# Performance work log

Measured on AMD Instinct MI355X. Metric: run time of the kernel, lower is better.

Reference implementation:

```python
import jax, jax.numpy as jnp
import numpy as np

B, T, V, D, OUT = 32, 100, 10000, 128, 1000
CODE_P = 0.003  # ~30 active codes per visit


def gru_dir(x3, whh, bhh, reverse):
    """x3: [B,T,3F] precomputed input-side gates (W_ih x + b_ih). PyTorch GRU math."""
    F = whh.shape[1]
    h0 = jnp.zeros((x3.shape[0], F), x3.dtype)

    def step(h, xt):
        gh = h @ whh.T + bhh
        xr, xz, xn = jnp.split(xt, 3, -1)
        hr, hz, hn = jnp.split(gh, 3, -1)
        r = jax.nn.sigmoid(xr + hr)
        z = jax.nn.sigmoid(xz + hz)
        n = jnp.tanh(xn + r * hn)
        h_new = (1.0 - z) * n + z * h
        return h_new, h_new

    _, hs = jax.lax.scan(step, h0, jnp.swapaxes(x3, 0, 1), reverse=reverse)
    return jnp.swapaxes(hs, 0, 1)  # [B,T,F]


def setup_inputs() -> dict:
    key = jax.random.key(0)
    ks = jax.random.split(key, 16)
    s = lambda k, *sh: jax.random.normal(k, sh, dtype=jnp.float32) * 0.05
    # multi-hot visits, ~0/1 with density CODE_P; force code 0 present so no all-zero visit
    x = (jax.random.uniform(ks[0], (B, T, V)) < CODE_P).astype(jnp.float32)
    x = x.at[:, :, 0].set(1.0)
    return {
        "batchdata": x,
        "emb": s(ks[1], V, D),
        "wih_f": s(ks[2], 3 * D, D), "whh_f": s(ks[3], 3 * D, D),
        "bih_f": jnp.zeros((3 * D,), jnp.float32), "bhh_f": jnp.zeros((3 * D,), jnp.float32),
        "wih_b": s(ks[4], 3 * D, D), "whh_b": s(ks[5], 3 * D, D),
        "bih_b": jnp.zeros((3 * D,), jnp.float32), "bhh_b": jnp.zeros((3 * D,), jnp.float32),
        "attn_w": s(ks[6], 2 * D, 1), "attn_b": jnp.zeros((1,), jnp.float32),
        "comb_w": s(ks[7], D, 4 * D), "comb_b": jnp.zeros((D,), jnp.float32),
        "fc_w": s(ks[8], OUT, D), "fc_b": jnp.zeros((OUT,), jnp.float32),
    }


def reference(batchdata, emb, wih_f, whh_f, bih_f, bhh_f, wih_b, whh_b, bih_b, bhh_b,
              attn_w, attn_b, comb_w, comb_b, fc_w, fc_b):
    # multihot_to_embedding: sum of embedding rows where visit==1 == multihot @ table
    e = jnp.einsum('btv,vd->btd', batchdata, emb)          # [B,T,D]
    mask = jnp.any(e != 0, axis=2)                          # [B,T]
    # DipoleLayer: bidirectional GRU (hidden=D each dir), dropout in eval mode = identity
    xf = jnp.einsum('btf,gf->btg', e, wih_f) + bih_f
    xb = jnp.einsum('btf,gf->btg', e, wih_b) + bih_b
    hf = gru_dir(xf, whh_f, bhh_f, reverse=False)
    hb = gru_dir(xb, whh_b, bhh_b, reverse=True)
    h = jnp.concatenate([hf, hb], axis=-1)                  # [B,T,2D]
    # location-based attention over timesteps
    scores = (h @ attn_w)[..., 0] + attn_b[0]               # [B,T]
    scores = jnp.where(mask, scores, jnp.float32(-1e9))
    a = jax.nn.softmax(scores, axis=-1)
    c = jnp.einsum('bt,btf->bf', a, h)                      # [B,2D] context
    last = jnp.sum(mask.astype(jnp.int32), axis=-1) - 1     # last valid visit
    h_last = h[jnp.arange(h.shape[0]), last]                # [B,2D]
    feat = jnp.tanh(jnp.concatenate([c, h_last], -1) @ comb_w.T + comb_b)  # [B,D]
    logits = feat @ fc_w.T + fc_b                           # [B,OUT]
    return logits
```

## Files before the change

### kernel.cpp

```cpp
#include <hip/hip_runtime.h>
#include <hip/hip_fp16.h>
#include <math.h>

#define BB 32
#define TT 100
#define VV 10000
#define DD 128
#define OUTN 1000
#define G3 384

__global__ __launch_bounds__(256) void k_w2h(
    const float* __restrict__ wf, const float* __restrict__ wb,
    __half* __restrict__ hf, __half* __restrict__ hb)
{
    const int i = blockIdx.x * 256 + threadIdx.x;
    hf[i] = __float2half(wf[i]);
    hb[i] = __float2half(wb[i]);
}

__global__ __launch_bounds__(256) void k_embed(
    const float* __restrict__ x, const float* __restrict__ emb,
    float* __restrict__ e, int* __restrict__ mask)
{
    const int bt  = blockIdx.x;
    const int tid = threadIdx.x;
    __shared__ int   s_cnt;
    __shared__ int   s_any;
    __shared__ int   s_idx[256];
    __shared__ float s_val[256];
    if (tid == 0) { s_cnt = 0; s_any = 0; }
    __syncthreads();

    const float4* x4 = (const float4*)(x + (size_t)bt * VV);
    for (int i = tid; i < VV / 4; i += 256) {
        float4 v = x4[i];
        if (v.x != 0.f) { int p = atomicAdd(&s_cnt, 1); if (p < 256) { s_idx[p] = 4*i+0; s_val[p] = v.x; } }
        if (v.y != 0.f) { int p = atomicAdd(&s_cnt, 1); if (p < 256) { s_idx[p] = 4*i+1; s_val[p] = v.y; } }
        if (v.z != 0.f) { int p = atomicAdd(&s_cnt, 1); if (p < 256) { s_idx[p] = 4*i+2; s_val[p] = v.z; } }
        if (v.w != 0.f) { int p = atomicAdd(&s_cnt, 1); if (p < 256) { s_idx[p] = 4*i+3; s_val[p] = v.w; } }
    }
    __syncthreads();
    int cnt = s_cnt; if (cnt > 256) cnt = 256;
    if (tid < DD) {
        float a0 = 0.f, a1 = 0.f, a2 = 0.f, a3 = 0.f;
        int i = 0;
        for (; i + 3 < cnt; i += 4) {
            a0 += s_val[i+0] * emb[(size_t)s_idx[i+0] * DD + tid];
            a1 += s_val[i+1] * emb[(size_t)s_idx[i+1] * DD + tid];
            a2 += s_val[i+2] * emb[(size_t)s_idx[i+2] * DD + tid];
            a3 += s_val[i+3] * emb[(size_t)s_idx[i+3] * DD + tid];
        }
        for (; i < cnt; ++i)
            a0 += s_val[i] * emb[(size_t)s_idx[i] * DD + tid];
        float acc = (a0 + a1) + (a2 + a3);
        e[(size_t)bt * DD + tid] = acc;
        if (acc != 0.f) s_any = 1;
    }
    __syncthreads();
    if (tid == 0) mask[bt] = s_any;
}

__global__ __launch_bounds__(256) void k_gates(
    const float* __restrict__ e,
    const float* __restrict__ wih_f, const float* __restrict__ bih_f,
    const float* __restrict__ wih_b, const float* __restrict__ bih_b,
    float* __restrict__ x3)
{
    const int r0  = blockIdx.x * 8;
    const int tid = threadIdx.x;
    __shared__ __align__(16) float se[8][DD];
    for (int i = tid; i < 8 * DD; i += 256)
        se[i >> 7][i & 127] = e[(size_t)(r0 + (i >> 7)) * DD + (i & 127)];
    __syncthreads();

    for (int cc = 0; cc < 3; ++cc) {
        const int col = tid + cc * 256;
        const float* wrow;
        float bias;
        if (col < G3) { wrow = wih_f + (size_t)col * DD;        bias = bih_f[col]; }
        else          { wrow = wih_b + (size_t)(col - G3) * DD; bias = bih_b[col - G3]; }
        float acc[8];
        #pragma unroll
        for (int r = 0; r < 8; ++r) acc[r] = 0.f;
        const float4* w4 = (const float4*)wrow;
        for (int k4 = 0; k4 < DD / 4; ++k4) {
            float4 w = w4[k4];
            #pragma unroll
            for (int r = 0; r < 8; ++r) {
                float4 ev = *(const float4*)&se[r][4 * k4];
                acc[r] += ev.x * w.x + ev.y * w.y + ev.z * w.z + ev.w * w.w;
            }
        }
        #pragma unroll
        for (int r = 0; r < 8; ++r)
            x3[(size_t)(r0 + r) * 768 + col] = acc[r] + bias;
    }
}

__device__ __forceinline__ uint4 ld_pin_u128(const uint4* p)
{
    uint4 r;
    asm volatile("global_load_dwordx4 %0, %1, off" : "=v"(r) : "v"(p));
    return r;
}

typedef _Float16 h2v __attribute__((ext_vector_type(2)));
__device__ __forceinline__ h2v u2h2(unsigned u) { h2v h; __builtin_memcpy(&h, &u, 4); return h; }
__device__ __forceinline__ float2 h2f2(unsigned u)
{
    __half2 h = *reinterpret_cast<__half2*>(&u);
    return __half22float2(h);
}

#if __has_builtin(__builtin_amdgcn_fdot2)
#define DOT2(acc, wu, hu) acc = __builtin_amdgcn_fdot2(u2h2(wu), u2h2(hu), acc, false);
#else
#define DOT2(acc, wu, hu) { float2 wf_ = h2f2(wu); float2 hf_ = h2f2(hu); acc += wf_.x*hf_.x + wf_.y*hf_.y; }
#endif

__global__ __launch_bounds__(512, 1) void k_gru(
    const float* __restrict__ x3,
    const __half* __restrict__ whh16_f, const float* __restrict__ bhh_f,
    const __half* __restrict__ whh16_b, const float* __restrict__ bhh_b,
    float* __restrict__ h_all)
{
    const int dir = blockIdx.x & 1;
    const int b   = blockIdx.x >> 1;
    const int tid = threadIdx.x;
    const int g   = tid & 127;
    const int kq  = tid >> 7;
    const int kb  = kq * 32;
    const __half* whh = dir ? whh16_b : whh16_f;
    const float*  bhh = dir ? bhh_b  : bhh_f;

    const uint4* pr4 = (const uint4*)(whh + (size_t)(g         ) * DD + kb);
    const uint4* pz4 = (const uint4*)(whh + (size_t)(DD     + g) * DD + kb);
    const uint4* pn4 = (const uint4*)(whh + (size_t)(2 * DD + g) * DD + kb);

#define Q4(M) M(0) M(1) M(2) M(3)
#define DECLW(j) uint4 wr##j = ld_pin_u128(pr4 + (j)); \
                 uint4 wz##j = ld_pin_u128(pz4 + (j)); \
                 uint4 wn##j = ld_pin_u128(pn4 + (j));
    Q4(DECLW)
#undef DECLW
    asm volatile("s_waitcnt vmcnt(0)" ::: "memory");
    __builtin_amdgcn_sched_barrier(0);

    float bhr = 0.f, bhz = 0.f, bhn = 0.f;
    if (tid < DD) { bhr = bhh[g]; bhz = bhh[DD + g]; bhn = bhh[2 * DD + g]; }

    __shared__ __align__(16) __half h16[DD];
    __shared__ float p_lds[9 * DD];
    float h_reg = 0.f;
    if (tid < DD) h16[tid] = __float2half(0.f);

    float xr = 0.f, xz = 0.f, xn = 0.f;
    {
        const float* x3p = x3 + (size_t)(b * TT + (dir ? TT - 1 : 0)) * 768 + dir * G3;
        if (tid < DD) { xr = x3p[g]; xz = x3p[DD + g]; xn = x3p[2 * DD + g]; }
    }
    __syncthreads();

    for (int t = 0; t < TT; ++t) {
        const int te = dir ? (TT - 1 - t) : t;

        float nxr = 0.f, nxz = 0.f, nxn = 0.f;
        if (t + 1 < TT) {
            const int tn = dir ? (TT - 2 - t) : (t + 1);
            const float* x3n = x3 + (size_t)(b * TT + tn) * 768 + dir * G3;
            if (tid < DD) { nxr = x3n[g]; nxz = x3n[DD + g]; nxn = x3n[2 * DD + g]; }
        }

        float ar0 = 0.f, ar1 = 0.f, az0 = 0.f, az1 = 0.f, an0 = 0.f, an1 = 0.f;
#define FMA8(j) { \
        const uint4 hv = *(const uint4*)&h16[kb + 8 * (j)]; \
        DOT2(ar0, wr##j.x, hv.x) DOT2(ar1, wr##j.y, hv.y) \
        DOT2(ar0, wr##j.z, hv.z) DOT2(ar1, wr##j.w, hv.w) \
        DOT2(az0, wz##j.x, hv.x) DOT2(az1, wz##j.y, hv.y) \
        DOT2(az0, wz##j.z, hv.z) DOT2(az1, wz##j.w, hv.w) \
        DOT2(an0, wn##j.x, hv.x) DOT2(an1, wn##j.y, hv.y) \
        DOT2(an0, wn##j.z, hv.z) DOT2(an1, wn##j.w, hv.w) }
        Q4(FMA8)
#undef FMA8
        const float pr = ar0 + ar1, pz = az0 + az1, pn = an0 + an1;

        if (kq) {
            const int q = (kq - 1) * 3;
            p_lds[(q + 0) * DD + g] = pr;
            p_lds[(q + 1) * DD + g] = pz;
            p_lds[(q + 2) * DD + g] = pn;
        }
        __syncthreads();

        if (tid < DD) {
            float hr = pr + p_lds[0*DD+g] + p_lds[3*DD+g] + p_lds[6*DD+g] + bhr;
            float hz = pz + p_lds[1*DD+g] + p_lds[4*DD+g] + p_lds[7*DD+g] + bhz;
            float hn = pn + p_lds[2*DD+g] + p_lds[5*DD+g] + p_lds[8*DD+g] + bhn;
            float r  = __builtin_amdgcn_rcpf(1.f + __expf(-(xr + hr)));
            float z  = __builtin_amdgcn_rcpf(1.f + __expf(-(xz + hz)));
            float e2 = __expf(2.f * (xn + r * hn));
            float n  = 1.f - 2.f * __builtin_amdgcn_rcpf(e2 + 1.f);
            float hnew = n + z * (h_reg - n);
            h_reg = hnew;
            h16[g] = __float2half(hnew);
            h_all[(size_t)((dir * BB + b) * TT + te) * DD + g] = hnew;
        }
        __syncthreads();
        xr = nxr; xz = nxz; xn = nxn;
    }
#undef Q4
}

__global__ __launch_bounds__(256) void k_attn(
    const float* __restrict__ h_all, const int* __restrict__ mask,
    const float* __restrict__ attn_w, const float* __restrict__ attn_b,
    const float* __restrict__ comb_w, const float* __restrict__ comb_b,
    float* __restrict__ feat)
{
    const int b   = blockIdx.x;
    const int tid = threadIdx.x;
    __shared__ float s_aw[256];
    __shared__ float s_sc[128];
    __shared__ int   s_m[128];
    __shared__ float s_red[128];
    __shared__ __align__(16) float s_ch[512];

    s_aw[tid] = attn_w[tid];
    int m = 0;
    if (tid < 128) {
        m = (tid < TT) ? mask[b * TT + tid] : 0;
        s_m[tid] = m;
    }
    __syncthreads();
    for (int s = 64; s > 0; s >>= 1) {
        if (tid < s) s_m[tid] += s_m[tid + s];
        __syncthreads();
    }
    const int last = s_m[0] - 1;

    const float* hf = h_all + (size_t)(0 * BB + b) * TT * DD;
    const float* hb = h_all + (size_t)(1 * BB + b) * TT * DD;

    float sc = -1e9f;
    if (tid < TT) {
        float a = attn_b[0];
        const float4* hf4 = (const float4*)(hf + (size_t)tid * DD);
        const float4* hb4 = (const float4*)(hb + (size_t)tid * DD);
        for (int k = 0; k < DD / 4; ++k) {
            float4 v = hf4[k];
            a += v.x * s_aw[4*k] + v.y * s_aw[4*k+1] + v.z * s_aw[4*k+2] + v.w * s_aw[4*k+3];
        }
        for (int k = 0; k < DD / 4; ++k) {
            float4 v = hb4[k];
            a += v.x * s_aw[DD+4*k] + v.y * s_aw[DD+4*k+1] + v.z * s_aw[DD+4*k+2] + v.w * s_aw[DD+4*k+3];
        }
        sc = m ? a : -1e9f;
    }
    if (tid < 128) { s_sc[tid] = sc; s_red[tid] = sc; }
    __syncthreads();
    for (int s = 64; s > 0; s >>= 1) {
        if (tid < s) s_red[tid] = fmaxf(s_red[tid], s_red[tid + s]);
        __syncthreads();
    }
    const float mx = s_red[0];
    __syncthreads();
    float ex = 0.f;
    if (tid < 128) { ex = __expf(s_sc[tid] - mx); s_sc[tid] = ex; s_red[tid] = ex; }
    __syncthreads();
    for (int s = 64; s > 0; s >>= 1) {
        if (tid < s) s_red[tid] += s_red[tid + s];
        __syncthreads();
    }
    const float inv = 1.f / s_red[0];
    __syncthreads();

    {
        const int fl = tid & 127;
        const float* hp = (tid < 128) ? hf : hb;
        float csum = 0.f;
        for (int t = 0; t < TT; ++t)
            csum += s_sc[t] * hp[(size_t)t * DD + fl];
        s_ch[tid]       = csum * inv;
        s_ch[256 + tid] = hp[(size_t)last * DD + fl];
    }
    __syncthreads();

    if (tid < 128) {
        float a = comb_b[tid];
        const float4* cw = (const float4*)(comb_w + (size_t)tid * 512);
        for (int k = 0; k < 128; ++k) {
            float4 w4 = cw[k];
            float4 v4 = *(const float4*)&s_ch[4 * k];
            a += w4.x * v4.x + w4.y * v4.y + w4.z * v4.z + w4.w * v4.w;
        }
        feat[(size_t)b * DD + tid] = tanhf(a);
    }
}

__global__ __launch_bounds__(256) void k_logits(
    const float* __restrict__ feat, const float* __restrict__ fc_w,
    const float* __restrict__ fc_b, float* __restrict__ out)
{
    const int b   = blockIdx.x >> 2;
    const int oc  = blockIdx.x & 3;
    const int tid = threadIdx.x;
    const int o   = oc * 256 + tid;
    __shared__ __align__(16) float s_f[DD];
    if (tid < DD) s_f[tid] = feat[(size_t)b * DD + tid];
    __syncthreads();
    if (o < OUTN) {
        float a = fc_b[o];
        const float4* w4 = (const float4*)(fc_w + (size_t)o * DD);
        for (int k = 0; k < DD / 4; ++k) {
            float4 w = w4[k];
            float4 v = *(const float4*)&s_f[4 * k];
            a += w.x * v.x + w.y * v.y + w.z * v.z + w.w * v.w;
        }
        out[(size_t)b * OUTN + o] = a;
    }
}

extern "C" void kernel_launch(void* const* d_in, const int* in_sizes, int n_in,
                              void* d_out, int out_size, void* d_ws, size_t ws_size,
                              hipStream_t stream)
{
    const float* x      = (const float*)d_in[0];
    const float* emb    = (const float*)d_in[1];
    const float* wih_f  = (const float*)d_in[2];
    const float* whh_f  = (const float*)d_in[3];
    const float* bih_f  = (const float*)d_in[4];
    const float* bhh_f  = (const float*)d_in[5];
    const float* wih_b  = (const float*)d_in[6];
    const float* whh_b  = (const float*)d_in[7];
    const float* bih_b  = (const float*)d_in[8];
    const float* bhh_b  = (const float*)d_in[9];
    const float* attn_w = (const float*)d_in[10];
    const float* attn_b = (const float*)d_in[11];
    const float* comb_w = (const float*)d_in[12];
    const float* comb_b = (const float*)d_in[13];
    const float* fc_w   = (const float*)d_in[14];
    const float* fc_b   = (const float*)d_in[15];
    float* out = (float*)d_out;

    float*  ws      = (float*)d_ws;
    float*  e       = ws;
    float*  x3      = ws + 409600;
    float*  h_all   = ws + 2867200;
    float*  feat    = ws + 3686400;
    int*    mask    = (int*)(ws + 3690496);
    __half* whh16_f = (__half*)(ws + 3693696);
    __half* whh16_b = (__half*)(ws + 3718272);

    k_w2h    <<<(3*DD*DD)/256, 256, 0, stream>>>(whh_f, whh_b, whh16_f, whh16_b);
    k_embed  <<<BB * TT,     256, 0, stream>>>(x, emb, e, mask);
    k_gates  <<<(BB * TT)/8, 256, 0, stream>>>(e, wih_f, bih_f, wih_b, bih_b, x3);
    k_gru    <<<2 * BB,      512, 0, stream>>>(x3, whh16_f, bhh_f, whh16_b, bhh_b, h_all);
    k_attn   <<<BB,          256, 0, stream>>>(h_all, mask, attn_w, attn_b, comb_w, comb_b, feat);
    k_logits <<<BB * 4,      256, 0, stream>>>(feat, fc_w, fc_b, out);
}
```

Baseline: 339.6 us.

## Collapse GRU k-split into single-wave-group blocks with double-buffered hidden state

The recurrent GRU kernel drops from 512 to 128 threads per block, with each thread computing the full 128-wide dot products for its gate column. This removes the LDS partial-sum reduction and one of the two barriers per timestep by double-buffering the fp16 hidden state. Recurrent weights are no longer pinned in registers but re-read from global memory/cache every timestep. Per-thread serial work on the latency-bound critical path quadruples.

```diff
diff --git a/kernel.cpp b/kernel.cpp
--- a/kernel.cpp
+++ b/kernel.cpp
@@ -97,13 +97,6 @@
     }
 }
 
-__device__ __forceinline__ uint4 ld_pin_u128(const uint4* p)
-{
-    uint4 r;
-    asm volatile("global_load_dwordx4 %0, %1, off" : "=v"(r) : "v"(p));
-    return r;
-}
-
 typedef _Float16 h2v __attribute__((ext_vector_type(2)));
 __device__ __forceinline__ h2v u2h2(unsigned u) { h2v h; __builtin_memcpy(&h, &u, 4); return h; }
 __device__ __forceinline__ float2 h2f2(unsigned u)
@@ -118,7 +111,7 @@
 #define DOT2(acc, wu, hu) { float2 wf_ = h2f2(wu); float2 hf_ = h2f2(hu); acc += wf_.x*hf_.x + wf_.y*hf_.y; }
 #endif
 
-__global__ __launch_bounds__(512, 1) void k_gru(
+__global__ __launch_bounds__(128, 1) void k_gru(
     const float* __restrict__ x3,
     const __half* __restrict__ whh16_f, const float* __restrict__ bhh_f,
     const __half* __restrict__ whh16_b, const float* __restrict__ bhh_b,
@@ -126,41 +119,28 @@
 {
     const int dir = blockIdx.x & 1;
     const int b   = blockIdx.x >> 1;
-    const int tid = threadIdx.x;
-    const int g   = tid & 127;
-    const int kq  = tid >> 7;
-    const int kb  = kq * 32;
+    const int g   = threadIdx.x;
     const __half* whh = dir ? whh16_b : whh16_f;
     const float*  bhh = dir ? bhh_b  : bhh_f;
 
-    const uint4* pr4 = (const uint4*)(whh + (size_t)(g         ) * DD + kb);
-    const uint4* pz4 = (const uint4*)(whh + (size_t)(DD     + g) * DD + kb);
-    const uint4* pn4 = (const uint4*)(whh + (size_t)(2 * DD + g) * DD + kb);
-
-#define Q4(M) M(0) M(1) M(2) M(3)
-#define DECLW(j) uint4 wr##j = ld_pin_u128(pr4 + (j)); \
-                 uint4 wz##j = ld_pin_u128(pz4 + (j)); \
-                 uint4 wn##j = ld_pin_u128(pn4 + (j));
-    Q4(DECLW)
-#undef DECLW
-    asm volatile("s_waitcnt vmcnt(0)" ::: "memory");
-    __builtin_amdgcn_sched_barrier(0);
-
-    float bhr = 0.f, bhz = 0.f, bhn = 0.f;
-    if (tid < DD) { bhr = bhh[g]; bhz = bhh[DD + g]; bhn = bhh[2 * DD + g]; }
-
-    __shared__ __align__(16) __half h16[DD];
-    __shared__ float p_lds[9 * DD];
+    const uint4* pr = (const uint4*)(whh + (size_t)(g         ) * DD);
+    const uint4* pz = (const uint4*)(whh + (size_t)(DD     + g) * DD);
+    const uint4* pn = (const uint4*)(whh + (size_t)(2 * DD + g) * DD);
+
+    const float bhr = bhh[g], bhz = bhh[DD + g], bhn = bhh[2 * DD + g];
+
+    __shared__ __align__(16) __half h16[2][DD];
     float h_reg = 0.f;
-    if (tid < DD) h16[tid] = __float2half(0.f);
-
-    float xr = 0.f, xz = 0.f, xn = 0.f;
+    h16[0][g] = __float2half(0.f);
+
+    float xr, xz, xn;
     {
         const float* x3p = x3 + (size_t)(b * TT + (dir ? TT - 1 : 0)) * 768 + dir * G3;
-        if (tid < DD) { xr = x3p[g]; xz = x3p[DD + g]; xn = x3p[2 * DD + g]; }
-    }
-    __syncthreads();
-
+        xr = x3p[g]; xz = x3p[DD + g]; xn = x3p[2 * DD + g];
+    }
+    __syncthreads();
+
+    int cur = 0;
     for (int t = 0; t < TT; ++t) {
         const int te = dir ? (TT - 1 - t) : t;
 
@@ -168,47 +148,41 @@
         if (t + 1 < TT) {
             const int tn = dir ? (TT - 2 - t) : (t + 1);
             const float* x3n = x3 + (size_t)(b * TT + tn) * 768 + dir * G3;
-            if (tid < DD) { nxr = x3n[g]; nxz = x3n[DD + g]; nxn = x3n[2 * DD + g]; }
-        }
-
+            nxr = x3n[g]; nxz = x3n[DD + g]; nxn = x3n[2 * DD + g];
+        }
+
+        const __half* hc = h16[cur];
         float ar0 = 0.f, ar1 = 0.f, az0 = 0.f, az1 = 0.f, an0 = 0.f, an1 = 0.f;
-#define FMA8(j) { \
-        const uint4 hv = *(const uint4*)&h16[kb + 8 * (j)]; \
-        DOT2(ar0, wr##j.x, hv.x) DOT2(ar1, wr##j.y, hv.y) \
-        DOT2(ar0, wr##j.z, hv.z) DOT2(ar1, wr##j.w, hv.w) \
-        DOT2(az0, wz##j.x, hv.x) DOT2(az1, wz##j.y, hv.y) \
-        DOT2(az0, wz##j.z, hv.z) DOT2(az1, wz##j.w, hv.w) \
-        DOT2(an0, wn##j.x, hv.x) DOT2(an1, wn##j.y, hv.y) \
-        DOT2(an0, wn##j.z, hv.z) DOT2(an1, wn##j.w, hv.w) }
-        Q4(FMA8)
-#undef FMA8
-        const float pr = ar0 + ar1, pz = az0 + az1, pn = an0 + an1;
-
-        if (kq) {
-            const int q = (kq - 1) * 3;
-            p_lds[(q + 0) * DD + g] = pr;
-            p_lds[(q + 1) * DD + g] = pz;
-            p_lds[(q + 2) * DD + g] = pn;
-        }
+        #pragma unroll
+        for (int j = 0; j < 16; ++j) {
+            const uint4 hv = *(const uint4*)&hc[8 * j];
+            const uint4 wr = pr[j];
+            const uint4 wz = pz[j];
+            const uint4 wn = pn[j];
+            DOT2(ar0, wr.x, hv.x) DOT2(ar1, wr.y, hv.y)
+            DOT2(ar0, wr.z, hv.z) DOT2(ar1, wr.w, hv.w)
+            DOT2(az0, wz.x, hv.x) DOT2(az1, wz.y, hv.y)
+            DOT2(az0, wz.z, hv.z) DOT2(az1, wz.w, hv.w)
+            DOT2(an0, wn.x, hv.x) DOT2(an1, wn.y, hv.y)
+            DOT2(an0, wn.z, hv.z) DOT2(an1, wn.w, hv.w)
+        }
+
+        const float hr = ar0 + ar1 + bhr;
+        const float hz = az0 + az1 + bhz;
+        const float hn = an0 + an1 + bhn;
+        const float r  = __builtin_amdgcn_rcpf(1.f + __expf(-(xr + hr)));
+        const float z  = __builtin_amdgcn_rcpf(1.f + __expf(-(xz + hz)));
+        const float e2 = __expf(2.f * (xn + r * hn));
+        const float n  = 1.f - 2.f * __builtin_amdgcn_rcpf(e2 + 1.f);
+        const float hnew = n + z * (h_reg - n);
+        h_reg = hnew;
+        h16[cur ^ 1][g] = __float2half(hnew);
+        h_all[(size_t)((dir * BB + b) * TT + te) * DD + g] = hnew;
+
         __syncthreads();
-
-        if (tid < DD) {
-            float hr = pr + p_lds[0*DD+g] + p_lds[3*DD+g] + p_lds[6*DD+g] + bhr;
-            float hz = pz + p_lds[1*DD+g] + p_lds[4*DD+g] + p_lds[7*DD+g] + bhz;
-            float hn = pn + p_lds[2*DD+g] + p_lds[5*DD+g] + p_lds[8*DD+g] + bhn;
-            float r  = __builtin_amdgcn_rcpf(1.f + __expf(-(xr + hr)));
-            float z  = __builtin_amdgcn_rcpf(1.f + __expf(-(xz + hz)));
-            float e2 = __expf(2.f * (xn + r * hn));
-            float n  = 1.f - 2.f * __builtin_amdgcn_rcpf(e2 + 1.f);
-            float hnew = n + z * (h_reg - n);
-            h_reg = hnew;
-            h16[g] = __float2half(hnew);
-            h_all[(size_t)((dir * BB + b) * TT + te) * DD + g] = hnew;
-        }
-        __syncthreads();
+        cur ^= 1;
         xr = nxr; xz = nxz; xn = nxn;
     }
-#undef Q4
 }
 
 __global__ __launch_bounds__(256) void k_attn(
@@ -354,7 +328,7 @@
     k_w2h    <<<(3*DD*DD)/256, 256, 0, stream>>>(whh_f, whh_b, whh16_f, whh16_b);
     k_embed  <<<BB * TT,     256, 0, stream>>>(x, emb, e, mask);
     k_gates  <<<(BB * TT)/8, 256, 0, stream>>>(e, wih_f, bih_f, wih_b, bih_b, x3);
-    k_gru    <<<2 * BB,      512, 0, stream>>>(x3, whh16_f, bhh_f, whh16_b, bhh_b, h_all);
+    k_gru    <<<2 * BB,      128, 0, stream>>>(x3, whh16_f, bhh_f, whh16_b, bhh_b, h_all);
     k_attn   <<<BB,          256, 0, stream>>>(h_all, mask, attn_w, attn_b, comb_w, comb_b, feat);
     k_logits <<<BB * 4,      256, 0, stream>>>(feat, fc_w, fc_b, out);
 }
```

Result: slower. 349.2 us (+2.8%).
